# Optimization experiments

Hardware: AMD Instinct MI355X
Metric: run time of the kernel (lower is better)

## Reference

```python
import jax, jax.numpy as jnp
import numpy as np

HEADS = 10
L1, L2 = 3.0, 3.0
OBS_X, OBS_Y = 0.0, 7.0
R = 4.0


def _forward(x, mean, std, mean_label, std_label,
             W1, b1, W2, b2, W31, b31, W32, b32,
             W41, b41, W42, b42, W51, b51, W52, b52, wt):
    relu = jax.nn.relu
    B = x.shape[0]
    x0 = x * std + mean  # unnormalized state (theta1, w1, theta2, w2)
    # multi-branch MLP
    h1 = relu(x @ W1.T + b1)
    h2 = relu(h1 @ W2.T + b2)
    h31 = relu(h2 @ W31.T + b31)
    h32 = relu(h2 @ W32.T + b32)
    h41 = relu(h31 @ W41.T + b41)
    h42 = relu(h32 @ W42.T + b42)
    x51 = h41 @ W51.T + b51                      # (B, 2*HEADS) per-head refs
    x52 = 4.0 * jax.nn.sigmoid(h42 @ W52.T + b52)  # (B, HEADS+1) CBF class-K gains

    th1, w1v, th2, w2v = x0[:, 0], x0[:, 1], x0[:, 2], x0[:, 3]
    s1, c1 = jnp.sin(th1), jnp.cos(th1)
    s2, c2 = jnp.sin(th2), jnp.cos(th2)
    px = L1 * c1 + L2 * c2 - OBS_X
    py = L1 * s1 + L2 * s2 - OBS_Y
    vx = -L1 * s1 * w1v - L2 * s2 * w2v
    vy = L1 * c1 * w1v + L2 * c2 * w2v
    barrier = px * px + py * py - R * R
    b_dot = 2.0 * px * vx + 2.0 * py * vy
    Lf2b = (2.0 * vx * vx + 2.0 * vy * vy
            + 2.0 * px * (-L1 * c1 * w1v ** 2 - L2 * c2 * w2v ** 2)
            + 2.0 * py * (-L1 * s1 * w1v ** 2 - L2 * s2 * w2v ** 2))
    g1 = 2.0 * px * (-L1 * s1) + 2.0 * py * (L1 * c1)
    g2 = 2.0 * px * (-L2 * s2) + 2.0 * py * (L2 * c2)
    G = -jnp.stack([g1, g2], axis=1)  # (B, 2), single inequality row per sample

    ref = jnp.transpose(x51.reshape(B, HEADS, 2), (1, 0, 2))  # (HEADS, B, 2)
    alpha = x52[:, 0:1]           # (B, 1)
    betas = x52[:, 1:]            # (B, HEADS)
    # h[k, b] = Lf2b + (a+bk)*b_dot + a*bk*barrier
    h = (Lf2b[:, None] + (alpha + betas) * b_dot[:, None]
         + alpha * betas * barrier[:, None]).T  # (HEADS, B)

    # QP: min 0.5||u||^2 + ref^T u  s.t.  G u <= h   (Q = I, 1 constraint)
    # closed form: u = -ref - max(0, (G.(-ref) - h)/(G.G)) * G
    u_unc = -ref                                  # (HEADS, B, 2)
    Gdot = jnp.sum(G * G, axis=1)                 # (B,)
    viol = jnp.einsum('hbc,bc->hb', u_unc, G) - h
    lam = jnp.maximum(viol / Gdot[None, :], 0.0)
    sol = u_unc - lam[..., None] * G[None, :, :]  # (HEADS, B, 2)

    wv = jax.nn.softmax(wt)                       # (HEADS,)
    rt = jnp.einsum('h,hbc->bc', wv, sol)         # (B, 2)
    return (rt - mean_label) / std_label


def setup_inputs() -> dict:
    key = jax.random.key(0)
    B = 16384
    dims = [4, 2048, 2048, 1024, 1024, 1024, 1024, 2]
    ks = jax.random.split(key, 10)

    def lin(k, fin, fout):
        kw, kb = jax.random.split(k)
        W = jax.random.normal(kw, (fout, fin), jnp.float32) / jnp.sqrt(float(fin))
        b = 0.01 * jax.random.normal(kb, (fout,), jnp.float32)
        return W, b

    W1, b1 = lin(ks[0], dims[0], dims[1])
    W2, b2 = lin(ks[1], dims[1], dims[2])
    W31, b31 = lin(ks[2], dims[2], dims[3])
    W32, b32 = lin(ks[3], dims[2], dims[4])
    W41, b41 = lin(ks[4], dims[3], dims[5])
    W42, b42 = lin(ks[5], dims[4], dims[6])
    W51, b51 = lin(ks[6], dims[5], dims[7] * HEADS)
    W52, b52 = lin(ks[7], dims[6], HEADS + 1)
    wt = jnp.ones((HEADS,), jnp.float32)
    x = jax.random.normal(ks[8], (B, dims[0]), jnp.float32)
    return {
        'x': x, 'sgn': 1,
        'mean': jnp.zeros((4,), jnp.float32), 'std': jnp.ones((4,), jnp.float32),
        'mean_label': jnp.zeros((2,), jnp.float32), 'std_label': jnp.ones((2,), jnp.float32),
        'W1': W1, 'b1': b1, 'W2': W2, 'b2': b2, 'W31': W31, 'b31': b31,
        'W32': W32, 'b32': b32, 'W41': W41, 'b41': b41, 'W42': W42, 'b42': b42,
        'W51': W51, 'b51': b51, 'W52': W52, 'b52': b52, 'wt': wt,
    }


def reference(x, sgn, mean, std, mean_label, std_label,
              W1, b1, W2, b2, W31, b31, W32, b32,
              W41, b41, W42, b42, W51, b51, W52, b52, wt):
    del sgn  # unused in the training (batched QP) path
    return _forward(x, mean, std, mean_label, std_label,
                    W1, b1, W2, b2, W31, b31, W32, b32,
                    W41, b41, W42, b42, W51, b51, W52, b52, wt)
```

## Files before the change

### kernel.cpp

```cpp
#include <hip/hip_runtime.h>

typedef unsigned short u16;
typedef unsigned char  u8;
typedef unsigned int   u32;
typedef __attribute__((ext_vector_type(8)))  short short8;
typedef __attribute__((ext_vector_type(16))) float floatx16;
typedef __attribute__((ext_vector_type(4)))  int   intx4;
typedef __attribute__((ext_vector_type(16))) int   intx16;
typedef __attribute__((ext_vector_type(8)))  u16   u16x8;
typedef __attribute__((ext_vector_type(4)))  u16   u16x4;

__device__ __forceinline__ u16 f2b(float f) {
    u32 u = __float_as_uint(f);
    u = (u + 0x7FFFu + ((u >> 16) & 1u)) >> 16;
    return (u16)u;
}
__device__ __forceinline__ float b2f(u16 h) {
    return __uint_as_float(((u32)h) << 16);
}
__device__ __forceinline__ int q8(float v, float inv) {
    return __float2int_rn(fminf(fmaxf(v * inv, -127.f), 127.f));
}

__device__ __forceinline__ void pad_block(const float* __restrict__ Wsrc, int rows,
                                          u16* __restrict__ Wdst,
                                          const float* __restrict__ bsrc,
                                          float* __restrict__ bdst, int blk) {
    int i = blk * 256 + threadIdx.x;
    int idx = i * 4;
    int r = idx >> 10;
    int c = idx & 1023;
    u16x4 o;
    if (r < rows) {
        float4 v = *(const float4*)&Wsrc[r * 1024 + c];
        o[0] = f2b(v.x); o[1] = f2b(v.y); o[2] = f2b(v.z); o[3] = f2b(v.w);
    } else {
        o[0] = 0; o[1] = 0; o[2] = 0; o[3] = 0;
    }
    *(u16x4*)&Wdst[idx] = o;
    if (i < 128) bdst[i] = (i < rows) ? bsrc[i] : 0.f;
}

__device__ __forceinline__ void wquant_row(const float* __restrict__ src,
                                           int K, u8* __restrict__ dstrow,
                                           float* __restrict__ sW,
                                           float* __restrict__ Wsum, int row_out) {
    const int lane = threadIdx.x & 63;
    const int iters = K >> 8;
    float mx = 0.f;
    for (int i = 0; i < iters; ++i) {
        float4 v = *(const float4*)&src[i * 256 + lane * 4];
        mx = fmaxf(mx, fmaxf(fmaxf(fabsf(v.x), fabsf(v.y)),
                             fmaxf(fabsf(v.z), fabsf(v.w))));
    }
#pragma unroll
    for (int off = 32; off >= 1; off >>= 1) mx = fmaxf(mx, __shfl_xor(mx, off));
    float sw  = fmaxf(mx * (1.f / 127.f), 1e-20f);
    float inv = 1.f / sw;
    int ssum = 0;
    for (int i = 0; i < iters; ++i) {
        float4 v = *(const float4*)&src[i * 256 + lane * 4];
        int q0 = q8(v.x, inv), q1 = q8(v.y, inv), q2 = q8(v.z, inv), q3 = q8(v.w, inv);
        ssum += q0 + q1 + q2 + q3;
        u32 p = (q0 & 255) | ((q1 & 255) << 8) | ((q2 & 255) << 16) | ((q3 & 255) << 24);
        *(u32*)&dstrow[i * 256 + lane * 4] = p;
    }
#pragma unroll
    for (int off = 32; off >= 1; off >>= 1) ssum += __shfl_xor(ssum, off);
    if (lane == 0) { sW[row_out] = sw; Wsum[row_out] = sw * (float)ssum; }
}

__device__ __forceinline__ void l1q_block(const float* __restrict__ x,
                                          const float* __restrict__ W1,
                                          const float* __restrict__ b1,
                                          u8* __restrict__ h1q,
                                          float* __restrict__ sA,
                                          float* __restrict__ muA, int blk) {
    __shared__ float wmx[4], wmn[4];
    const int t    = threadIdx.x;
    const int wave = t >> 6;
    const int lane = t & 63;
    const int b0 = blk * 16;
    const int n0 = t * 8;
    float4 wreg[8]; float breg[8];
    const float4* W14 = (const float4*)W1;
#pragma unroll
    for (int i = 0; i < 8; ++i) { wreg[i] = W14[n0 + i]; breg[i] = b1[n0 + i]; }
    for (int r = 0; r < 16; ++r) {
        int b = b0 + r;
        float4 xv = ((const float4*)x)[b];
        float v[8];
        float lmx = 0.f, lmn = 3.4e38f;
#pragma unroll
        for (int i = 0; i < 8; ++i) {
            float s = xv.x * wreg[i].x + xv.y * wreg[i].y +
                      xv.z * wreg[i].z + xv.w * wreg[i].w + breg[i];
            s = fmaxf(s, 0.f);
            v[i] = s;
            lmx = fmaxf(lmx, s); lmn = fminf(lmn, s);
        }
#pragma unroll
        for (int off = 32; off >= 1; off >>= 1) {
            lmx = fmaxf(lmx, __shfl_xor(lmx, off));
            lmn = fminf(lmn, __shfl_xor(lmn, off));
        }
        if (lane == 0) { wmx[wave] = lmx; wmn[wave] = lmn; }
        __syncthreads();
        float mx = fmaxf(fmaxf(wmx[0], wmx[1]), fmaxf(wmx[2], wmx[3]));
        float mn = fminf(fminf(wmn[0], wmn[1]), fminf(wmn[2], wmn[3]));
        float mu  = 0.5f * (mx + mn);
        float s   = fmaxf((mx - mn) * (1.f / 254.f), 1e-20f);
        float inv = 1.f / s;
        int q[8];
#pragma unroll
        for (int i = 0; i < 8; ++i) q[i] = q8(v[i] - mu, inv);
        uint2 p;
        p.x = (q[0] & 255) | ((q[1] & 255) << 8) | ((q[2] & 255) << 16) | ((q[3] & 255) << 24);
        p.y = (q[4] & 255) | ((q[5] & 255) << 8) | ((q[6] & 255) << 16) | ((q[7] & 255) << 24);
        *(uint2*)&h1q[(size_t)b * 2048 + n0] = p;
        if (t == 0) { sA[b] = s; muA[b] = mu; }
        __syncthreads();
    }
}

__global__ __launch_bounds__(256)
void k_prep1(const float* W2, u8* W2q, float* sW2, float* Wsum2,
             const float* x, const float* W1, const float* b1,
             u8* h1q, float* sA1, float* muA1) {
    int blk = blockIdx.x;
    if (blk < 512) {
        int row = blk * 4 + (threadIdx.x >> 6);
        wquant_row(W2 + (size_t)row * 2048, 2048, W2q + (size_t)row * 2048,
                   sW2, Wsum2, row);
        return;
    }
    l1q_block(x, W1, b1, h1q, sA1, muA1, blk - 512);
}

template<int NCH>
__global__ __launch_bounds__(256)
void k_aquant(const u16* __restrict__ src, u8* __restrict__ dst,
              float* __restrict__ s, float* __restrict__ mu) {
    const int wave = threadIdx.x >> 6;
    const int lane = threadIdx.x & 63;
    const int row  = blockIdx.x * 4 + wave;
    const int rowlen = NCH * 512;
    const u16* sr = src + (size_t)row * rowlen;
    u8*       dr  = dst + (size_t)row * rowlen;
    u16x8 vbuf[NCH];
    float mx = -3.4e38f, mn = 3.4e38f;
#pragma unroll
    for (int c = 0; c < NCH; ++c) {
        u16x8 v = *(const u16x8*)&sr[c * 512 + lane * 8];
        vbuf[c] = v;
#pragma unroll
        for (int i = 0; i < 8; ++i) {
            float f = b2f(v[i]);
            mx = fmaxf(mx, f); mn = fminf(mn, f);
        }
    }
#pragma unroll
    for (int off = 32; off >= 1; off >>= 1) {
        mx = fmaxf(mx, __shfl_xor(mx, off));
        mn = fminf(mn, __shfl_xor(mn, off));
    }
    float m  = 0.5f * (mx + mn);
    float sc = fmaxf((mx - mn) * (1.f / 254.f), 1e-20f);
    float inv = 1.f / sc;
#pragma unroll
    for (int c = 0; c < NCH; ++c) {
        u16x8 v = vbuf[c];
        int q[8];
#pragma unroll
        for (int i = 0; i < 8; ++i) q[i] = q8(b2f(v[i]) - m, inv);
        uint2 p;
        p.x = (q[0] & 255) | ((q[1] & 255) << 8) | ((q[2] & 255) << 16) | ((q[3] & 255) << 24);
        p.y = (q[4] & 255) | ((q[5] & 255) << 8) | ((q[6] & 255) << 16) | ((q[7] & 255) << 24);
        *(uint2*)&dr[c * 512 + lane * 8] = p;
    }
    if (lane == 0) { s[row] = sc; mu[row] = m; }
}

__device__ __forceinline__ void backfill_prep(
        int pblk,
        const float* W31, const float* W32, u8* W3q, float* sW3, float* Wsum3,
        const float* W41, u8* W41q, float* sW41, float* Ws41,
        const float* W42, u8* W42q, float* sW42, float* Ws42,
        const float* W51, u16* W51p, const float* b51, float* b51p,
        const float* W52, u16* W52p, const float* b52, float* b52p,
        const float* b31, const float* b32, float* b3c) {
    if (pblk < 512) {
        int row = pblk * 4 + (threadIdx.x >> 6);
        const float* src = (row < 1024) ? W31 + (size_t)row * 2048
                                        : W32 + (size_t)(row - 1024) * 2048;
        wquant_row(src, 2048, W3q + (size_t)row * 2048, sW3, Wsum3, row);
        return;
    }
    pblk -= 512;
    if (pblk < 256) {
        int row = pblk * 4 + (threadIdx.x >> 6);
        wquant_row(W41 + (size_t)row * 1024, 1024, W41q + (size_t)row * 1024,
                   sW41, Ws41, row);
        return;
    }
    pblk -= 256;
    if (pblk < 256) {
        int row = pblk * 4 + (threadIdx.x >> 6);
        wquant_row(W42 + (size_t)row * 1024, 1024, W42q + (size_t)row * 1024,
                   sW42, Ws42, row);
        return;
    }
    pblk -= 256;
    if (pblk < 128) { pad_block(W51, 20, W51p, b51, b51p, pblk); return; }
    pblk -= 128;
    if (pblk < 128) { pad_block(W52, 11, W52p, b52, b52p, pblk); return; }
    pblk -= 128;
    if (pblk < 8) {
        int i = pblk * 256 + threadIdx.x;
        b3c[i] = (i < 1024) ? b31[i] : b32[i - 1024];
    }
}

__global__ __launch_bounds__(256, 2)
void k_gemmq(const u8* __restrict__ A, const u8* __restrict__ Wq,
             const float* __restrict__ sA, const float* __restrict__ muA,
             const float* __restrict__ sW, const float* __restrict__ Wsum,
             const float* __restrict__ bias, u16* __restrict__ C,
             int K, int lda, int ldc, int sstride, int gemmY,
             const u8* A2, const u8* Wq2,
             const float* sA2, const float* muA2,
             const float* sW2, const float* Wsum2,
             const float* bias2, u16* C2, int split,
             const float* W31, const float* W32, u8* W3q, float* sW3, float* Wsum3,
             const float* W41, u8* W41q, float* sW41, float* Ws41,
             const float* W42, u8* W42q, float* sW42, float* Ws42,
             const float* W51, u16* W51p, const float* b51, float* b51p,
             const float* W52, u16* W52p, const float* b52, float* b52p,
             const float* b31, const float* b32, float* b3c) {
    const int ngemm = gemmY * gridDim.x;
    int flat = blockIdx.y * gridDim.x + blockIdx.x;
    if (flat >= ngemm) {
        backfill_prep(flat - ngemm, W31, W32, W3q, sW3, Wsum3,
                      W41, W41q, sW41, Ws41, W42, W42q, sW42, Ws42,
                      W51, W51p, b51, b51p, W52, W52p, b52, b52p,
                      b31, b32, b3c);
        return;
    }

    __shared__ __align__(16) u8 As[256 * 128];
    __shared__ __align__(16) u8 Ws[128 * 128];

    const int tid  = threadIdx.x;
    const int wave = tid >> 6;
    const int lane = tid & 63;

    int xcd = flat & 7;
    int p   = flat >> 3;
    int bx  = p % gridDim.x;
    int by  = (p / gridDim.x) * 8 + xcd;
    if (A2 != nullptr && by >= split) {
        A = A2; Wq = Wq2; sA = sA2; muA = muA2; sW = sW2; Wsum = Wsum2;
        bias = bias2; C = C2; by -= split;
    }
    const int bm = by * 256;
    const int bn = bx * 128;

    const int srow = lane >> 3;
    const int sg   = ((lane & 7) ^ srow) * 16;

    const int wm    = (wave & 1) * 128;
    const int wn    = (wave >> 1) * 64;
    const int row32 = lane & 31;
    const int half  = lane >> 5;

    intx16 acc[4][2];
#pragma unroll
    for (int i = 0; i < 4; ++i)
#pragma unroll
        for (int j = 0; j < 2; ++j)
#pragma unroll
            for (int r = 0; r < 16; ++r) acc[i][j][r] = 0;

    for (int k0 = 0; k0 < K; k0 += 128) {
#pragma unroll
        for (int i = 0; i < 8; ++i) {
            int ci = wave * 8 + i;
            int r  = ci * 8 + srow;
            const u8* ga = A + (size_t)(bm + r) * lda + k0 + sg;
            __builtin_amdgcn_global_load_lds(
                (const __attribute__((address_space(1))) void*)ga,
                (__attribute__((address_space(3))) void*)&As[ci * 1024], 16, 0, 0);
        }
#pragma unroll
        for (int i = 0; i < 4; ++i) {
            int ci = wave * 4 + i;
            int r  = ci * 8 + srow;
            const u8* gw = Wq + (size_t)(bn + r) * K + k0 + sg;
            __builtin_amdgcn_global_load_lds(
                (const __attribute__((address_space(1))) void*)gw,
                (__attribute__((address_space(3))) void*)&Ws[ci * 1024], 16, 0, 0);
        }
        __syncthreads();

#pragma unroll
        for (int s = 0; s < 4; ++s) {
            const int c = s * 2 + half;
            intx4 af[4], bf[2];
#pragma unroll
            for (int i = 0; i < 4; ++i) {
                int r = wm + i * 32 + row32;
                af[i] = *(const intx4*)&As[r * 128 + ((c ^ (r & 7)) * 16)];
            }
#pragma unroll
            for (int j = 0; j < 2; ++j) {
                int r = wn + j * 32 + row32;
                bf[j] = *(const intx4*)&Ws[r * 128 + ((c ^ (r & 7)) * 16)];
            }
#pragma unroll
            for (int i = 0; i < 4; ++i)
#pragma unroll
                for (int j = 0; j < 2; ++j)
                    acc[i][j] = __builtin_amdgcn_mfma_i32_32x32x32_i8(
                        af[i], bf[j], acc[i][j], 0, 0, 0);
        }
        __syncthreads();
    }

    float sWv[2], Wsv[2], bv[2];
#pragma unroll
    for (int j = 0; j < 2; ++j) {
        int col = bn + wn + j * 32 + row32;
        sWv[j] = sW[col]; Wsv[j] = Wsum[col]; bv[j] = bias[col];
    }
#pragma unroll
    for (int i = 0; i < 4; ++i)
#pragma unroll
        for (int r = 0; r < 16; ++r) {
            int row = bm + wm + i * 32 + (r & 3) + 8 * (r >> 2) + 4 * half;
            float sa = sA[row * sstride], mu = muA[row * sstride];
#pragma unroll
            for (int j = 0; j < 2; ++j) {
                int col = bn + wn + j * 32 + row32;
                float v = (float)acc[i][j][r] * (sa * sWv[j]) + mu * Wsv[j] + bv[j];
                v = fmaxf(v, 0.f);
                C[(size_t)row * ldc + col] = f2b(v);
            }
        }
}

__global__ __launch_bounds__(256, 2)
void k_heads_final(const u16* __restrict__ hbuf,
                   const u16* __restrict__ W51p, const float* __restrict__ b51p,
                   const u16* __restrict__ W52p, const float* __restrict__ b52p,
                   const float* __restrict__ x, const float* __restrict__ mean,
                   const float* __restrict__ std_,
                   const float* __restrict__ mean_label,
                   const float* __restrict__ std_label,
                   const float* __restrict__ wt, float* __restrict__ out) {
    __shared__ __align__(16) u16 As[128 * 64];
    __shared__ __align__(16) u16 Ws[128 * 64];
    __shared__ float x51s[128 * 20];
    __shared__ float x52s[128 * 11];

    const int tid  = threadIdx.x;
    const int wave = tid >> 6;
    const int lane = tid & 63;
    const int bm   = blockIdx.x * 128;

    const int srow = lane >> 3;
    const int sg   = ((lane & 7) ^ srow) * 8;

    const int wm    = (wave & 1) * 64;
    const int wn    = (wave >> 1) * 64;
    const int row32 = lane & 31;
    const int half  = lane >> 5;

    auto run_gemm = [&](const u16* Abase, const u16* Wp, const float* bp,
                        float* dst, int ncols) {
        floatx16 acc[2][2];
#pragma unroll
        for (int i = 0; i < 2; ++i)
#pragma unroll
            for (int j = 0; j < 2; ++j)
#pragma unroll
                for (int r = 0; r < 16; ++r) acc[i][j][r] = 0.f;

        for (int k0 = 0; k0 < 1024; k0 += 64) {
#pragma unroll
            for (int i = 0; i < 4; ++i) {
                int ci = wave * 4 + i;
                int r  = ci * 8 + srow;
                const u16* ga = Abase + (size_t)(bm + r) * 2048 + k0 + sg;
                __builtin_amdgcn_global_load_lds(
                    (const __attribute__((address_space(1))) void*)ga,
                    (__attribute__((address_space(3))) void*)&As[ci * 512], 16, 0, 0);
                const u16* gw = Wp + (size_t)r * 1024 + k0 + sg;
                __builtin_amdgcn_global_load_lds(
                    (const __attribute__((address_space(1))) void*)gw,
                    (__attribute__((address_space(3))) void*)&Ws[ci * 512], 16, 0, 0);
            }
            __syncthreads();
#pragma unroll
            for (int s = 0; s < 4; ++s) {
                const int c = s * 2 + half;
                short8 a0, a1, b0, b1;
                { int r = wm + row32;       a0 = *(const short8*)&As[r * 64 + ((c ^ (r & 7)) * 8)]; }
                { int r = wm + 32 + row32;  a1 = *(const short8*)&As[r * 64 + ((c ^ (r & 7)) * 8)]; }
                { int r = wn + row32;       b0 = *(const short8*)&Ws[r * 64 + ((c ^ (r & 7)) * 8)]; }
                { int r = wn + 32 + row32;  b1 = *(const short8*)&Ws[r * 64 + ((c ^ (r & 7)) * 8)]; }
                acc[0][0] = __builtin_amdgcn_mfma_f32_32x32x16_bf16(a0, b0, acc[0][0], 0, 0, 0);
                acc[0][1] = __builtin_amdgcn_mfma_f32_32x32x16_bf16(a0, b1, acc[0][1], 0, 0, 0);
                acc[1][0] = __builtin_amdgcn_mfma_f32_32x32x16_bf16(a1, b0, acc[1][0], 0, 0, 0);
                acc[1][1] = __builtin_amdgcn_mfma_f32_32x32x16_bf16(a1, b1, acc[1][1], 0, 0, 0);
            }
            __syncthreads();
        }
#pragma unroll
        for (int i = 0; i < 2; ++i)
#pragma unroll
            for (int j = 0; j < 2; ++j) {
                int col = wn + j * 32 + row32;
                if (col < ncols) {
                    float bj = bp[col];
#pragma unroll
                    for (int r = 0; r < 16; ++r) {
                        int row = wm + i * 32 + (r & 3) + 8 * (r >> 2) + 4 * half;
                        dst[row * ncols + col] = acc[i][j][r] + bj;
                    }
                }
            }
    };

    run_gemm(hbuf,        W51p, b51p, x51s, 20);
    run_gemm(hbuf + 1024, W52p, b52p, x52s, 11);
    __syncthreads();

    if (tid < 128) {
        int b = bm + tid;

        float w[10], m = -1e30f;
#pragma unroll
        for (int h = 0; h < 10; ++h) { w[h] = wt[h]; m = fmaxf(m, w[h]); }
        float ssum = 0.f;
#pragma unroll
        for (int h = 0; h < 10; ++h) { w[h] = __expf(w[h] - m); ssum += w[h]; }
        float winv = 1.f / ssum;

        float4 xv = ((const float4*)x)[b];
        float th1 = xv.x * std_[0] + mean[0];
        float w1v = xv.y * std_[1] + mean[1];
        float th2 = xv.z * std_[2] + mean[2];
        float w2v = xv.w * std_[3] + mean[3];
        float s1 = sinf(th1), c1 = cosf(th1);
        float s2 = sinf(th2), c2 = cosf(th2);
        float px = 3.f * c1 + 3.f * c2 - 0.f;
        float py = 3.f * s1 + 3.f * s2 - 7.f;
        float vx = -3.f * s1 * w1v - 3.f * s2 * w2v;
        float vy =  3.f * c1 * w1v + 3.f * c2 * w2v;
        float barrier = px * px + py * py - 16.f;
        float b_dot = 2.f * (px * vx + py * vy);
        float Lf2b = 2.f * vx * vx + 2.f * vy * vy
                   + 2.f * px * (-3.f * c1 * w1v * w1v - 3.f * c2 * w2v * w2v)
                   + 2.f * py * (-3.f * s1 * w1v * w1v - 3.f * s2 * w2v * w2v);
        float g1 = 2.f * px * (-3.f * s1) + 2.f * py * (3.f * c1);
        float g2 = 2.f * px * (-3.f * s2) + 2.f * py * (3.f * c2);
        float Gx = -g1, Gy = -g2;
        float Gdot = Gx * Gx + Gy * Gy;

        float alpha = 4.f / (1.f + expf(-x52s[tid * 11 + 0]));

        float rx = 0.f, ry = 0.f;
#pragma unroll
        for (int h = 0; h < 10; ++h) {
            float r0 = x51s[tid * 20 + 2 * h];
            float r1 = x51s[tid * 20 + 2 * h + 1];
            float beta = 4.f / (1.f + expf(-x52s[tid * 11 + 1 + h]));
            float hh = Lf2b + (alpha + beta) * b_dot + alpha * beta * barrier;
            float ux = -r0, uy = -r1;
            float viol = ux * Gx + uy * Gy - hh;
            float lam = fmaxf(viol / Gdot, 0.f);
            float sx = ux - lam * Gx;
            float sy = uy - lam * Gy;
            float wk = w[h] * winv;
            rx += wk * sx; ry += wk * sy;
        }
        out[2 * b]     = (rx - mean_label[0]) / std_label[0];
        out[2 * b + 1] = (ry - mean_label[1]) / std_label[1];
    }
}

extern "C" void kernel_launch(void* const* d_in, const int* in_sizes, int n_in,
                              void* d_out, int out_size, void* d_ws, size_t ws_size,
                              hipStream_t stream) {
    const float* x    = (const float*)d_in[0];
    const float* mean = (const float*)d_in[2];
    const float* std_ = (const float*)d_in[3];
    const float* mean_label = (const float*)d_in[4];
    const float* std_label  = (const float*)d_in[5];
    const float* W1  = (const float*)d_in[6];
    const float* b1  = (const float*)d_in[7];
    const float* W2  = (const float*)d_in[8];
    const float* b2  = (const float*)d_in[9];
    const float* W31 = (const float*)d_in[10];
    const float* b31 = (const float*)d_in[11];
    const float* W32 = (const float*)d_in[12];
    const float* b32 = (const float*)d_in[13];
    const float* W41 = (const float*)d_in[14];
    const float* b41 = (const float*)d_in[15];
    const float* W42 = (const float*)d_in[16];
    const float* b42 = (const float*)d_in[17];
    const float* W51 = (const float*)d_in[18];
    const float* b51 = (const float*)d_in[19];
    const float* W52 = (const float*)d_in[20];
    const float* b52 = (const float*)d_in[21];
    const float* wt  = (const float*)d_in[22];

    const int B = in_sizes[0] / 4;

    char* wsp = (char*)d_ws;
    size_t off = 0;
    auto alloc = [&](size_t bytes) {
        void* p = wsp + off;
        off += (bytes + 255) & ~(size_t)255;
        return p;
    };
    u8*    W2q   = (u8*)   alloc((size_t)2048 * 2048);
    float* sW2   = (float*)alloc(2048 * 4);
    float* Wsum2 = (float*)alloc(2048 * 4);
    u8*    h1q   = (u8*)   alloc((size_t)B * 2048);
    float* sA1   = (float*)alloc((size_t)B * 4);
    float* muA1  = (float*)alloc((size_t)B * 4);
    u8*    W3q   = (u8*)   alloc((size_t)2048 * 2048);
    float* sW3   = (float*)alloc(2048 * 4);
    float* Wsum3 = (float*)alloc(2048 * 4);
    u8*    W41q  = (u8*)   alloc((size_t)1024 * 1024);
    float* sW41  = (float*)alloc(1024 * 4);
    float* Ws41  = (float*)alloc(1024 * 4);
    u8*    W42q  = (u8*)   alloc((size_t)1024 * 1024);
    float* sW42  = (float*)alloc(1024 * 4);
    float* Ws42  = (float*)alloc(1024 * 4);
    u16*   W51p  = (u16*)  alloc((size_t)128 * 1024 * 2);
    u16*   W52p  = (u16*)  alloc((size_t)128 * 1024 * 2);
    float* b51p  = (float*)alloc(512);
    float* b52p  = (float*)alloc(512);
    float* b3c   = (float*)alloc(2048 * 4);
    u8*    h2q   = (u8*)   alloc((size_t)B * 2048);
    float* s2a   = (float*)alloc((size_t)B * 4);
    float* mu2a  = (float*)alloc((size_t)B * 4);
    u8*    h34q  = (u8*)   alloc((size_t)B * 2048);
    float* s34   = (float*)alloc((size_t)2 * B * 4);
    float* mu34  = (float*)alloc((size_t)2 * B * 4);
    u16*   bufA  = (u16*)  alloc((size_t)B * 2048 * 2);
    u16*   bufB  = (u16*)  alloc((size_t)B * 2048 * 2);
    const u8* NUL8 = nullptr;

    k_prep1<<<1536, 256, 0, stream>>>(W2, W2q, sW2, Wsum2,
                                      x, W1, b1, h1q, sA1, muA1);

    k_gemmq<<<dim3(16, 64 + 81), 256, 0, stream>>>(
        h1q, W2q, sA1, muA1, sW2, Wsum2, b2, bufB, 2048, 2048, 2048, 1, 64,
        NUL8, NUL8, nullptr, nullptr, nullptr, nullptr, nullptr, nullptr, 0,
        W31, W32, W3q, sW3, Wsum3,
        W41, W41q, sW41, Ws41, W42, W42q, sW42, Ws42,
        W51, W51p, b51, b51p, W52, W52p, b52, b52p, b31, b32, b3c);

    k_aquant<4><<<B / 4, 256, 0, stream>>>(bufB, h2q, s2a, mu2a);

    k_gemmq<<<dim3(16, 64), 256, 0, stream>>>(
        h2q, W3q, s2a, mu2a, sW3, Wsum3, b3c, bufA, 2048, 2048, 2048, 1, 64,
        NUL8, NUL8, nullptr, nullptr, nullptr, nullptr, nullptr, nullptr, 0,
        nullptr, nullptr, nullptr, nullptr, nullptr,
        nullptr, nullptr, nullptr, nullptr, nullptr, nullptr, nullptr, nullptr,
        nullptr, nullptr, nullptr, nullptr, nullptr, nullptr, nullptr, nullptr,
        nullptr, nullptr, nullptr);

    k_aquant<2><<<2 * B / 4, 256, 0, stream>>>(bufA, h34q, s34, mu34);

    k_gemmq<<<dim3(8, 128), 256, 0, stream>>>(
        h34q, W41q, s34, mu34, sW41, Ws41, b41, bufB,
        1024, 2048, 2048, 2, 128,
        h34q + 1024, W42q, s34 + 1, mu34 + 1, sW42, Ws42, b42, bufB + 1024, 64,
        nullptr, nullptr, nullptr, nullptr, nullptr,
        nullptr, nullptr, nullptr, nullptr, nullptr, nullptr, nullptr, nullptr,
        nullptr, nullptr, nullptr, nullptr, nullptr, nullptr, nullptr, nullptr,
        nullptr, nullptr, nullptr);

    k_heads_final<<<B / 128, 256, 0, stream>>>(
        bufB, W51p, b51p, W52p, b52p, x, mean, std_,
        mean_label, std_label, wt, (float*)d_out);
}
```

Before: 409.6 us.

## Move weight prep into prep kernel and run both head GEMMs concurrently

```diff
diff --git a/kernel.cpp b/kernel.cpp
--- a/kernel.cpp
+++ b/kernel.cpp
@@ -126,7 +126,13 @@
 __global__ __launch_bounds__(256)
 void k_prep1(const float* W2, u8* W2q, float* sW2, float* Wsum2,
              const float* x, const float* W1, const float* b1,
-             u8* h1q, float* sA1, float* muA1) {
+             u8* h1q, float* sA1, float* muA1,
+             const float* W31, const float* W32, u8* W3q, float* sW3, float* Wsum3,
+             const float* W41, u8* W41q, float* sW41, float* Ws41,
+             const float* W42, u8* W42q, float* sW42, float* Ws42,
+             const float* W51, u16* W51p, const float* b51, float* b51p,
+             const float* W52, u16* W52p, const float* b52, float* b52p,
+             const float* b31, const float* b32, float* b3c) {
     int blk = blockIdx.x;
     if (blk < 512) {
         int row = blk * 4 + (threadIdx.x >> 6);
@@ -134,7 +140,39 @@
                    sW2, Wsum2, row);
         return;
     }
-    l1q_block(x, W1, b1, h1q, sA1, muA1, blk - 512);
+    blk -= 512;
+    if (blk < 1024) { l1q_block(x, W1, b1, h1q, sA1, muA1, blk); return; }
+    blk -= 1024;
+    if (blk < 512) {
+        int row = blk * 4 + (threadIdx.x >> 6);
+        const float* src = (row < 1024) ? W31 + (size_t)row * 2048
+                                        : W32 + (size_t)(row - 1024) * 2048;
+        wquant_row(src, 2048, W3q + (size_t)row * 2048, sW3, Wsum3, row);
+        return;
+    }
+    blk -= 512;
+    if (blk < 256) {
+        int row = blk * 4 + (threadIdx.x >> 6);
+        wquant_row(W41 + (size_t)row * 1024, 1024, W41q + (size_t)row * 1024,
+                   sW41, Ws41, row);
+        return;
+    }
+    blk -= 256;
+    if (blk < 256) {
+        int row = blk * 4 + (threadIdx.x >> 6);
+        wquant_row(W42 + (size_t)row * 1024, 1024, W42q + (size_t)row * 1024,
+                   sW42, Ws42, row);
+        return;
+    }
+    blk -= 256;
+    if (blk < 128) { pad_block(W51, 20, W51p, b51, b51p, blk); return; }
+    blk -= 128;
+    if (blk < 128) { pad_block(W52, 11, W52p, b52, b52p, blk); return; }
+    blk -= 128;
+    if (blk < 8) {
+        int i = blk * 256 + threadIdx.x;
+        b3c[i] = (i < 1024) ? b31[i] : b32[i - 1024];
+    }
 }
 
 template<int NCH>
@@ -181,72 +219,16 @@
     if (lane == 0) { s[row] = sc; mu[row] = m; }
 }
 
-__device__ __forceinline__ void backfill_prep(
-        int pblk,
-        const float* W31, const float* W32, u8* W3q, float* sW3, float* Wsum3,
-        const float* W41, u8* W41q, float* sW41, float* Ws41,
-        const float* W42, u8* W42q, float* sW42, float* Ws42,
-        const float* W51, u16* W51p, const float* b51, float* b51p,
-        const float* W52, u16* W52p, const float* b52, float* b52p,
-        const float* b31, const float* b32, float* b3c) {
-    if (pblk < 512) {
-        int row = pblk * 4 + (threadIdx.x >> 6);
-        const float* src = (row < 1024) ? W31 + (size_t)row * 2048
-                                        : W32 + (size_t)(row - 1024) * 2048;
-        wquant_row(src, 2048, W3q + (size_t)row * 2048, sW3, Wsum3, row);
-        return;
-    }
-    pblk -= 512;
-    if (pblk < 256) {
-        int row = pblk * 4 + (threadIdx.x >> 6);
-        wquant_row(W41 + (size_t)row * 1024, 1024, W41q + (size_t)row * 1024,
-                   sW41, Ws41, row);
-        return;
-    }
-    pblk -= 256;
-    if (pblk < 256) {
-        int row = pblk * 4 + (threadIdx.x >> 6);
-        wquant_row(W42 + (size_t)row * 1024, 1024, W42q + (size_t)row * 1024,
-                   sW42, Ws42, row);
-        return;
-    }
-    pblk -= 256;
-    if (pblk < 128) { pad_block(W51, 20, W51p, b51, b51p, pblk); return; }
-    pblk -= 128;
-    if (pblk < 128) { pad_block(W52, 11, W52p, b52, b52p, pblk); return; }
-    pblk -= 128;
-    if (pblk < 8) {
-        int i = pblk * 256 + threadIdx.x;
-        b3c[i] = (i < 1024) ? b31[i] : b32[i - 1024];
-    }
-}
-
 __global__ __launch_bounds__(256, 2)
 void k_gemmq(const u8* __restrict__ A, const u8* __restrict__ Wq,
              const float* __restrict__ sA, const float* __restrict__ muA,
              const float* __restrict__ sW, const float* __restrict__ Wsum,
              const float* __restrict__ bias, u16* __restrict__ C,
-             int K, int lda, int ldc, int sstride, int gemmY,
+             int K, int lda, int ldc, int sstride,
              const u8* A2, const u8* Wq2,
              const float* sA2, const float* muA2,
              const float* sW2, const float* Wsum2,
-             const float* bias2, u16* C2, int split,
-             const float* W31, const float* W32, u8* W3q, float* sW3, float* Wsum3,
-             const float* W41, u8* W41q, float* sW41, float* Ws41,
-             const float* W42, u8* W42q, float* sW42, float* Ws42,
-             const float* W51, u16* W51p, const float* b51, float* b51p,
-             const float* W52, u16* W52p, const float* b52, float* b52p,
-             const float* b31, const float* b32, float* b3c) {
-    const int ngemm = gemmY * gridDim.x;
-    int flat = blockIdx.y * gridDim.x + blockIdx.x;
-    if (flat >= ngemm) {
-        backfill_prep(flat - ngemm, W31, W32, W3q, sW3, Wsum3,
-                      W41, W41q, sW41, Ws41, W42, W42q, sW42, Ws42,
-                      W51, W51p, b51, b51p, W52, W52p, b52, b52p,
-                      b31, b32, b3c);
-        return;
-    }
-
+             const float* bias2, u16* C2, int split) {
     __shared__ __align__(16) u8 As[256 * 128];
     __shared__ __align__(16) u8 Ws[128 * 128];
 
@@ -254,6 +236,7 @@
     const int wave = tid >> 6;
     const int lane = tid & 63;
 
+    int flat = blockIdx.y * gridDim.x + blockIdx.x;
     int xcd = flat & 7;
     int p   = flat >> 3;
     int bx  = p % gridDim.x;
@@ -357,8 +340,9 @@
                    const float* __restrict__ mean_label,
                    const float* __restrict__ std_label,
                    const float* __restrict__ wt, float* __restrict__ out) {
-    __shared__ __align__(16) u16 As[128 * 64];
-    __shared__ __align__(16) u16 Ws[128 * 64];
+    __shared__ __align__(16) u16 A1[128 * 64];
+    __shared__ __align__(16) u16 A2[128 * 64];
+    __shared__ __align__(16) u16 Wl[2][32 * 64];
     __shared__ float x51s[128 * 20];
     __shared__ float x52s[128 * 11];
 
@@ -370,69 +354,71 @@
     const int srow = lane >> 3;
     const int sg   = ((lane & 7) ^ srow) * 8;
 
+    const int g     = wave >> 1;
     const int wm    = (wave & 1) * 64;
-    const int wn    = (wave >> 1) * 64;
     const int row32 = lane & 31;
     const int half  = lane >> 5;
 
-    auto run_gemm = [&](const u16* Abase, const u16* Wp, const float* bp,
-                        float* dst, int ncols) {
-        floatx16 acc[2][2];
-#pragma unroll
-        for (int i = 0; i < 2; ++i)
-#pragma unroll
-            for (int j = 0; j < 2; ++j)
-#pragma unroll
-                for (int r = 0; r < 16; ++r) acc[i][j][r] = 0.f;
-
-        for (int k0 = 0; k0 < 1024; k0 += 64) {
+    const u16* Abase = hbuf + (g ? 1024 : 0);
+    const u16* Wp    = g ? W52p : W51p;
+    u16* Asl = g ? A2 : A1;
+
+    floatx16 acc[2];
+#pragma unroll
+    for (int i = 0; i < 2; ++i)
+#pragma unroll
+        for (int r = 0; r < 16; ++r) acc[i][r] = 0.f;
+
+    for (int k0 = 0; k0 < 1024; k0 += 64) {
+#pragma unroll
+        for (int i = 0; i < 8; ++i) {
+            int rl = wm + i * 8 + srow;
+            const u16* ga = Abase + (size_t)(bm + rl) * 2048 + k0 + sg;
+            __builtin_amdgcn_global_load_lds(
+                (const __attribute__((address_space(1))) void*)ga,
+                (__attribute__((address_space(3))) void*)&Asl[(wm + i * 8) * 64],
+                16, 0, 0);
+        }
+        if ((wave & 1) == 0) {
 #pragma unroll
             for (int i = 0; i < 4; ++i) {
-                int ci = wave * 4 + i;
-                int r  = ci * 8 + srow;
-                const u16* ga = Abase + (size_t)(bm + r) * 2048 + k0 + sg;
-                __builtin_amdgcn_global_load_lds(
-                    (const __attribute__((address_space(1))) void*)ga,
-                    (__attribute__((address_space(3))) void*)&As[ci * 512], 16, 0, 0);
+                int r = i * 8 + srow;
                 const u16* gw = Wp + (size_t)r * 1024 + k0 + sg;
                 __builtin_amdgcn_global_load_lds(
                     (const __attribute__((address_space(1))) void*)gw,
-                    (__attribute__((address_space(3))) void*)&Ws[ci * 512], 16, 0, 0);
+                    (__attribute__((address_space(3))) void*)&Wl[g][(i * 8) * 64],
+                    16, 0, 0);
             }
-            __syncthreads();
-#pragma unroll
-            for (int s = 0; s < 4; ++s) {
-                const int c = s * 2 + half;
-                short8 a0, a1, b0, b1;
-                { int r = wm + row32;       a0 = *(const short8*)&As[r * 64 + ((c ^ (r & 7)) * 8)]; }
-                { int r = wm + 32 + row32;  a1 = *(const short8*)&As[r * 64 + ((c ^ (r & 7)) * 8)]; }
-                { int r = wn + row32;       b0 = *(const short8*)&Ws[r * 64 + ((c ^ (r & 7)) * 8)]; }
-                { int r = wn + 32 + row32;  b1 = *(const short8*)&Ws[r * 64 + ((c ^ (r & 7)) * 8)]; }
-                acc[0][0] = __builtin_amdgcn_mfma_f32_32x32x16_bf16(a0, b0, acc[0][0], 0, 0, 0);
-                acc[0][1] = __builtin_amdgcn_mfma_f32_32x32x16_bf16(a0, b1, acc[0][1], 0, 0, 0);
-                acc[1][0] = __builtin_amdgcn_mfma_f32_32x32x16_bf16(a1, b0, acc[1][0], 0, 0, 0);
-                acc[1][1] = __builtin_amdgcn_mfma_f32_32x32x16_bf16(a1, b1, acc[1][1], 0, 0, 0);
-            }
-            __syncthreads();
-        }
-#pragma unroll
-        for (int i = 0; i < 2; ++i)
-#pragma unroll
-            for (int j = 0; j < 2; ++j) {
-                int col = wn + j * 32 + row32;
-                if (col < ncols) {
-                    float bj = bp[col];
-#pragma unroll
-                    for (int r = 0; r < 16; ++r) {
-                        int row = wm + i * 32 + (r & 3) + 8 * (r >> 2) + 4 * half;
-                        dst[row * ncols + col] = acc[i][j][r] + bj;
-                    }
+        }
+        __syncthreads();
+#pragma unroll
+        for (int s = 0; s < 4; ++s) {
+            const int c = s * 2 + half;
+            short8 a0, a1, bf;
+            { int r = wm + row32;       a0 = *(const short8*)&Asl[r * 64 + ((c ^ (r & 7)) * 8)]; }
+            { int r = wm + 32 + row32;  a1 = *(const short8*)&Asl[r * 64 + ((c ^ (r & 7)) * 8)]; }
+            { int r = row32;            bf = *(const short8*)&Wl[g][r * 64 + ((c ^ (r & 7)) * 8)]; }
+            acc[0] = __builtin_amdgcn_mfma_f32_32x32x16_bf16(a0, bf, acc[0], 0, 0, 0);
+            acc[1] = __builtin_amdgcn_mfma_f32_32x32x16_bf16(a1, bf, acc[1], 0, 0, 0);
+        }
+        __syncthreads();
+    }
+
+    {
+        int col = row32;
+        int ncols = g ? 11 : 20;
+        if (col < ncols) {
+            float bj = (g ? b52p : b51p)[col];
+            float* dst = g ? x52s : x51s;
+#pragma unroll
+            for (int i = 0; i < 2; ++i)
+#pragma unroll
+                for (int r = 0; r < 16; ++r) {
+                    int row = wm + i * 32 + (r & 3) + 8 * (r >> 2) + 4 * half;
+                    dst[row * ncols + col] = acc[i][r] + bj;
                 }
-            }
-    };
-
-    run_gemm(hbuf,        W51p, b51p, x51s, 20);
-    run_gemm(hbuf + 1024, W52p, b52p, x52s, 11);
+        }
+    }
     __syncthreads();
 
     if (tid < 128) {
@@ -554,36 +540,28 @@
     u16*   bufB  = (u16*)  alloc((size_t)B * 2048 * 2);
     const u8* NUL8 = nullptr;
 
-    k_prep1<<<1536, 256, 0, stream>>>(W2, W2q, sW2, Wsum2,
-                                      x, W1, b1, h1q, sA1, muA1);
-
-    k_gemmq<<<dim3(16, 64 + 81), 256, 0, stream>>>(
-        h1q, W2q, sA1, muA1, sW2, Wsum2, b2, bufB, 2048, 2048, 2048, 1, 64,
-        NUL8, NUL8, nullptr, nullptr, nullptr, nullptr, nullptr, nullptr, 0,
+    k_prep1<<<2824, 256, 0, stream>>>(
+        W2, W2q, sW2, Wsum2, x, W1, b1, h1q, sA1, muA1,
         W31, W32, W3q, sW3, Wsum3,
         W41, W41q, sW41, Ws41, W42, W42q, sW42, Ws42,
         W51, W51p, b51, b51p, W52, W52p, b52, b52p, b31, b32, b3c);
 
+    k_gemmq<<<dim3(16, 64), 256, 0, stream>>>(
+        h1q, W2q, sA1, muA1, sW2, Wsum2, b2, bufB, 2048, 2048, 2048, 1,
+        NUL8, NUL8, nullptr, nullptr, nullptr, nullptr, nullptr, nullptr, 0);
+
     k_aquant<4><<<B / 4, 256, 0, stream>>>(bufB, h2q, s2a, mu2a);
 
     k_gemmq<<<dim3(16, 64), 256, 0, stream>>>(
-        h2q, W3q, s2a, mu2a, sW3, Wsum3, b3c, bufA, 2048, 2048, 2048, 1, 64,
-        NUL8, NUL8, nullptr, nullptr, nullptr, nullptr, nullptr, nullptr, 0,
-        nullptr, nullptr, nullptr, nullptr, nullptr,
-        nullptr, nullptr, nullptr, nullptr, nullptr, nullptr, nullptr, nullptr,
-        nullptr, nullptr, nullptr, nullptr, nullptr, nullptr, nullptr, nullptr,
-        nullptr, nullptr, nullptr);
+        h2q, W3q, s2a, mu2a, sW3, Wsum3, b3c, bufA, 2048, 2048, 2048, 1,
+        NUL8, NUL8, nullptr, nullptr, nullptr, nullptr, nullptr, nullptr, 0);
 
     k_aquant<2><<<2 * B / 4, 256, 0, stream>>>(bufA, h34q, s34, mu34);
 
     k_gemmq<<<dim3(8, 128), 256, 0, stream>>>(
         h34q, W41q, s34, mu34, sW41, Ws41, b41, bufB,
-        1024, 2048, 2048, 2, 128,
-        h34q + 1024, W42q, s34 + 1, mu34 + 1, sW42, Ws42, b42, bufB + 1024, 64,
-        nullptr, nullptr, nullptr, nullptr, nullptr,
-        nullptr, nullptr, nullptr, nullptr, nullptr, nullptr, nullptr, nullptr,
-        nullptr, nullptr, nullptr, nullptr, nullptr, nullptr, nullptr, nullptr,
-        nullptr, nullptr, nullptr);
+        1024, 2048, 2048, 2,
+        h34q + 1024, W42q, s34 + 1, mu34 + 1, sW42, Ws42, b42, bufB + 1024, 64);
 
     k_heads_final<<<B / 128, 256, 0, stream>>>(
         bufB, W51p, b51p, W52p, b52p, x, mean, std_,
```

Result: no change. 402.9 us (-1.6%).
